# Kernel tuning notes

Measured on AMD Instinct MI355X. Metric: run time of the kernel, lower is better.

## Reference

```python
import jax, jax.numpy as jnp
import numpy as np

N_NODES = 50000
N_GRAPHS = 64


def _gcn_layer(x, w, b, src, dst, dinv):
    # GCNConv: out = D^{-1/2} (A+I) D^{-1/2} (x W) + b; self-loops already in src/dst
    xw = x @ w                                  # [N, out]
    norm = (dinv[src] * dinv[dst])[:, None]     # [E+N, 1]
    msgs = xw[src] * norm                       # gather + scale
    out = jax.ops.segment_sum(msgs, dst, num_segments=N_NODES)
    return out + b


def setup_inputs() -> dict:
    key = jax.random.key(0)
    ks = jax.random.split(key, 12)
    E = 800000
    F_IN, H = 128, 256
    x = jax.random.normal(ks[0], (N_NODES, F_IN), dtype=jnp.float32)
    edge_attr = jax.random.normal(ks[1], (E, 4), dtype=jnp.float32)
    edge_index = jax.random.randint(ks[2], (2, E), 0, N_NODES, dtype=jnp.int64)
    batch = jnp.sort(jax.random.randint(ks[3], (N_NODES,), 0, N_GRAPHS, dtype=jnp.int64))
    def glorot(k, fi, fo):
        s = jnp.sqrt(6.0 / (fi + fo))
        return jax.random.uniform(k, (fi, fo), minval=-s, maxval=s, dtype=jnp.float32)
    return {
        "x": x, "edge_attr": edge_attr, "edge_index": edge_index, "batch": batch,
        "w1": glorot(ks[4], F_IN, H), "b1": jnp.zeros((H,), jnp.float32),
        "w2": glorot(ks[5], H, H), "b2": jnp.zeros((H,), jnp.float32),
        "w3": glorot(ks[6], H, H), "b3": jnp.zeros((H,), jnp.float32),
        "lin1_w": glorot(ks[7], H, H // 2), "lin1_b": jnp.zeros((H // 2,), jnp.float32),
        "lin2_w": glorot(ks[8], H // 2, 3), "lin2_b": jnp.zeros((3,), jnp.float32),
    }


def reference(x, edge_attr, edge_index, batch, w1, b1, w2, b2, w3, b3,
              lin1_w, lin1_b, lin2_w, lin2_b):
    # add self-loops once; shared by all three conv layers
    loop = jnp.arange(N_NODES, dtype=edge_index.dtype)
    src = jnp.concatenate([edge_index[0], loop])
    dst = jnp.concatenate([edge_index[1], loop])
    deg = jax.ops.segment_sum(jnp.ones_like(dst, dtype=x.dtype), dst, num_segments=N_NODES)
    dinv = jnp.where(deg > 0, jax.lax.rsqrt(deg), 0.0)

    h = jax.nn.relu(_gcn_layer(x, w1, b1, src, dst, dinv))
    h = jax.nn.relu(_gcn_layer(h, w2, b2, src, dst, dinv))
    h = _gcn_layer(h, w3, b3, src, dst, dinv)

    # global mean pool over graphs
    sums = jax.ops.segment_sum(h, batch, num_segments=N_GRAPHS)
    cnts = jax.ops.segment_sum(jnp.ones((h.shape[0],), h.dtype), batch, num_segments=N_GRAPHS)
    pooled = sums / jnp.maximum(cnts, 1.0)[:, None]

    # eval mode: dropout is identity
    out = pooled @ lin1_w + lin1_b
    out = out @ lin2_w + lin2_b
    return out
```

## Files before the change

### kernel.cpp

```cpp
#include <hip/hip_runtime.h>
#include <cstdint>

constexpr int NG = 64;
constexpr int H  = 256;

__device__ __forceinline__ uint32_t pk_bf16(float a, float b) {
    uint32_t ua = __builtin_bit_cast(uint32_t, a);
    uint32_t ub = __builtin_bit_cast(uint32_t, b);
    ua += 0x7fffu + ((ua >> 16) & 1u);
    ub += 0x7fffu + ((ub >> 16) & 1u);
    return (ua >> 16) | (ub & 0xffff0000u);
}
__device__ __forceinline__ void bf2acc(uint32_t u, float& a0, float& a1) {
    a0 += __builtin_bit_cast(float, u << 16);
    a1 += __builtin_bit_cast(float, u & 0xffff0000u);
}

__global__ void hist_kernel(const int* __restrict__ dst, int* __restrict__ cnt, int E) {
    int e = blockIdx.x * blockDim.x + threadIdx.x;
    if (e < E) atomicAdd(&cnt[dst[e]], 1);
}

__global__ void dinv_kernel(const int* __restrict__ cnt, float* __restrict__ dinv, int n) {
    int i = blockIdx.x * blockDim.x + threadIdx.x;
    if (i < n) dinv[i] = rsqrtf((float)(cnt[i] + 1));
}

__global__ __launch_bounds__(256) void scanA(const int* __restrict__ cnt, int* __restrict__ bsum, int n) {
    __shared__ int sh[256];
    int t = threadIdx.x, i = blockIdx.x * 256 + t;
    sh[t] = (i < n) ? cnt[i] : 0;
    __syncthreads();
    for (int off = 128; off > 0; off >>= 1) {
        if (t < off) sh[t] += sh[t + off];
        __syncthreads();
    }
    if (t == 0) bsum[blockIdx.x] = sh[0];
}

__global__ __launch_bounds__(256) void scanB(const int* __restrict__ bsum, int* __restrict__ boff,
                                             int* __restrict__ total_out, int nb) {
    __shared__ int sh[256];
    int t = threadIdx.x;
    int v = (t < nb) ? bsum[t] : 0;
    sh[t] = v;
    __syncthreads();
    for (int off = 1; off < 256; off <<= 1) {
        int a = (t >= off) ? sh[t - off] : 0;
        __syncthreads();
        sh[t] += a;
        __syncthreads();
    }
    if (t < nb) boff[t] = sh[t] - v;
    if (t == nb - 1) *total_out = sh[t];
}

__global__ __launch_bounds__(256) void scanC(const int* __restrict__ cnt, const int* __restrict__ boff,
                                             int* __restrict__ row_ptr, int* __restrict__ fill, int n) {
    __shared__ int sh[256];
    int t = threadIdx.x, i = blockIdx.x * 256 + t;
    int v = (i < n) ? cnt[i] : 0;
    sh[t] = v;
    __syncthreads();
    for (int off = 1; off < 256; off <<= 1) {
        int a = (t >= off) ? sh[t - off] : 0;
        __syncthreads();
        sh[t] += a;
        __syncthreads();
    }
    if (i < n) {
        int excl = boff[blockIdx.x] + sh[t] - v;
        row_ptr[i] = excl;
        fill[i] = excl;
    }
}

__global__ void scatter_kernel(const int* __restrict__ src, const int* __restrict__ dst,
                               int* __restrict__ fill, int* __restrict__ ssrc, int E) {
    int e = blockIdx.x * blockDim.x + threadIdx.x;
    if (e < E) {
        int pos = atomicAdd(&fill[dst[e]], 1);
        ssrc[pos] = src[e];
    }
}

__global__ void prescale_kernel(const float* __restrict__ x, const float* __restrict__ dinv,
                                ushort* __restrict__ y, int total ) {
    int idx = blockIdx.x * blockDim.x + threadIdx.x;
    int f = idx * 4;
    if (f >= total) return;
    float dv = dinv[f >> 7];
    float4 v = *reinterpret_cast<const float4*>(x + f);
    uint2 o;
    o.x = pk_bf16(v.x * dv, v.y * dv);
    o.y = pk_bf16(v.z * dv, v.w * dv);
    *reinterpret_cast<uint2*>(y + f) = o;
}

template<int VEC>
__global__ __launch_bounds__(256) void agg_kernel(const ushort* __restrict__ y,
                                                  const float* __restrict__ dinv,
                                                  const int* __restrict__ row_ptr,
                                                  const int* __restrict__ ssrc,
                                                  float* __restrict__ z, int n) {
    constexpr int W = VEC * 64;
    int wave = threadIdx.x >> 6;
    int lane = threadIdx.x & 63;
    int node = blockIdx.x * 4 + wave;
    if (node >= n) return;
    float acc[VEC] = {};

    auto ld4 = [&](int s) -> uint2 {
        return *reinterpret_cast<const uint2*>(y + (size_t)s * W + lane * VEC);
    };
    auto ld2 = [&](int s) -> uint32_t {
        return *reinterpret_cast<const uint32_t*>(y + (size_t)s * W + lane * VEC);
    };

    if constexpr (VEC == 4) {
        uint2 v = ld4(node);
        bf2acc(v.x, acc[0], acc[1]); bf2acc(v.y, acc[2], acc[3]);
    } else {
        bf2acc(ld2(node), acc[0], acc[1]);
    }

    int beg = row_ptr[node], end = row_ptr[node + 1];
    int e = beg;
    for (; e + 4 <= end; e += 4) {
        int s0 = ssrc[e], s1 = ssrc[e + 1], s2 = ssrc[e + 2], s3 = ssrc[e + 3];
        if constexpr (VEC == 4) {
            uint2 v0 = ld4(s0), v1 = ld4(s1), v2 = ld4(s2), v3 = ld4(s3);
            bf2acc(v0.x, acc[0], acc[1]); bf2acc(v0.y, acc[2], acc[3]);
            bf2acc(v1.x, acc[0], acc[1]); bf2acc(v1.y, acc[2], acc[3]);
            bf2acc(v2.x, acc[0], acc[1]); bf2acc(v2.y, acc[2], acc[3]);
            bf2acc(v3.x, acc[0], acc[1]); bf2acc(v3.y, acc[2], acc[3]);
        } else {
            uint32_t v0 = ld2(s0), v1 = ld2(s1), v2 = ld2(s2), v3 = ld2(s3);
            bf2acc(v0, acc[0], acc[1]); bf2acc(v1, acc[0], acc[1]);
            bf2acc(v2, acc[0], acc[1]); bf2acc(v3, acc[0], acc[1]);
        }
    }
    for (; e < end; ++e) {
        if constexpr (VEC == 4) {
            uint2 v = ld4(ssrc[e]);
            bf2acc(v.x, acc[0], acc[1]); bf2acc(v.y, acc[2], acc[3]);
        } else {
            bf2acc(ld2(ssrc[e]), acc[0], acc[1]);
        }
    }

    float dv = dinv[node];
    float* zr = z + (size_t)node * W + lane * VEC;
    if constexpr (VEC == 4) {
        float4 o; o.x = dv * acc[0]; o.y = dv * acc[1]; o.z = dv * acc[2]; o.w = dv * acc[3];
        *reinterpret_cast<float4*>(zr) = o;
    } else {
        float2 o; o.x = dv * acc[0]; o.y = dv * acc[1];
        *reinterpret_cast<float2*>(zr) = o;
    }
}

template<bool RELU>
__global__ __launch_bounds__(256) void gemm_kernel(const float* __restrict__ A,
                                                   const float* __restrict__ Wm,
                                                   const float* __restrict__ bias,
                                                   const float* __restrict__ dinv,
                                                   ushort* __restrict__ C, int M, int K) {
    constexpr int BM = 64, BN = 64, BK = 32;
    __shared__ float As[BK][BM + 4];
    __shared__ float Bs[BK][BN];
    const int tid = threadIdx.x;
    const int bm = blockIdx.x * BM;
    const int bn = blockIdx.y * BN;
    const int tr = tid >> 4;
    const int tc = tid & 15;
    float acc[4][4] = {};
    for (int k0 = 0; k0 < K; k0 += BK) {
        #pragma unroll
        for (int i = tid; i < (BM * BK) / 4; i += 256) {
            int r = i >> 3;
            int c = (i & 7) << 2;
            float4 v = make_float4(0.f, 0.f, 0.f, 0.f);
            int grow = bm + r;
            if (grow < M) v = *reinterpret_cast<const float4*>(A + (size_t)grow * K + k0 + c);
            As[c + 0][r] = v.x; As[c + 1][r] = v.y; As[c + 2][r] = v.z; As[c + 3][r] = v.w;
        }
        #pragma unroll
        for (int i = tid; i < (BK * BN) / 4; i += 256) {
            int r = i >> 4;
            int c = (i & 15) << 2;
            *reinterpret_cast<float4*>(&Bs[r][c]) =
                *reinterpret_cast<const float4*>(Wm + (size_t)(k0 + r) * H + bn + c);
        }
        __syncthreads();
        #pragma unroll
        for (int kk = 0; kk < BK; ++kk) {
            float4 a = *reinterpret_cast<const float4*>(&As[kk][tr * 4]);
            float4 b = *reinterpret_cast<const float4*>(&Bs[kk][tc * 4]);
            float av[4] = {a.x, a.y, a.z, a.w};
            float bv[4] = {b.x, b.y, b.z, b.w};
            #pragma unroll
            for (int i = 0; i < 4; ++i)
                #pragma unroll
                for (int j = 0; j < 4; ++j)
                    acc[i][j] += av[i] * bv[j];
        }
        __syncthreads();
    }
    float4 bvals = *reinterpret_cast<const float4*>(bias + bn + tc * 4);
    float bb[4] = {bvals.x, bvals.y, bvals.z, bvals.w};
    #pragma unroll
    for (int i = 0; i < 4; ++i) {
        int row = bm + tr * 4 + i;
        if (row >= M) continue;
        float dv = dinv[row];
        float t0 = acc[i][0] + bb[0], t1 = acc[i][1] + bb[1];
        float t2 = acc[i][2] + bb[2], t3 = acc[i][3] + bb[3];
        if (RELU) { t0 = fmaxf(t0, 0.f); t1 = fmaxf(t1, 0.f); t2 = fmaxf(t2, 0.f); t3 = fmaxf(t3, 0.f); }
        uint2 o;
        o.x = pk_bf16(t0 * dv, t1 * dv);
        o.y = pk_bf16(t2 * dv, t3 * dv);
        *reinterpret_cast<uint2*>(C + (size_t)row * H + bn + tc * 4) = o;
    }
}

__global__ __launch_bounds__(256) void pool_kernel(const float* __restrict__ z,
                                                   const int* __restrict__ batch,
                                                   float* __restrict__ sums,
                                                   int* __restrict__ gcnt, int n) {
    constexpr int NCH = 128;
    int t = threadIdx.x;
    int base = blockIdx.x * NCH;
    if (base >= n) return;
    int endn = min(base + NCH, n);
    int cur = batch[base];
    float local = 0.f;
    int cl = 0;
    for (int i = base; i < endn; ++i) {
        int g = batch[i];
        if (g != cur) {
            atomicAdd(&sums[cur * H + t], local);
            if (t == 0) atomicAdd(&gcnt[cur], cl);
            local = 0.f; cl = 0; cur = g;
        }
        local += z[(size_t)i * H + t];
        cl++;
    }
    atomicAdd(&sums[cur * H + t], local);
    if (t == 0) atomicAdd(&gcnt[cur], cl);
}

__global__ __launch_bounds__(256) void head_kernel(const float* __restrict__ sums,
                                                   const int* __restrict__ gcnt,
                                                   const float* __restrict__ w3, const float* __restrict__ b3,
                                                   const float* __restrict__ l1w, const float* __restrict__ l1b,
                                                   const float* __restrict__ l2w, const float* __restrict__ l2b,
                                                   float* __restrict__ out) {
    __shared__ float pooled[H];
    __shared__ float t3[H];
    __shared__ float mid[H / 2];
    int g = blockIdx.x, t = threadIdx.x;
    float c = (float)max(gcnt[g], 1);
    pooled[t] = sums[g * H + t] / c;
    __syncthreads();
    float a = b3[t];
    for (int k = 0; k < H; ++k) a += pooled[k] * w3[k * H + t];
    t3[t] = a;
    __syncthreads();
    if (t < H / 2) {
        float m = l1b[t];
        for (int k = 0; k < H; ++k) m += t3[k] * l1w[k * (H / 2) + t];
        mid[t] = m;
    }
    __syncthreads();
    if (t < 3) {
        float o = l2b[t];
        for (int k = 0; k < H / 2; ++k) o += mid[k] * l2w[k * 3 + t];
        out[g * 3 + t] = o;
    }
}

extern "C" void kernel_launch(void* const* d_in, const int* in_sizes, int n_in,
                              void* d_out, int out_size, void* d_ws, size_t ws_size,
                              hipStream_t stream) {
    const float* x   = (const float*)d_in[0];
    const int*   ei  = (const int*)d_in[2];
    const int*   bat = (const int*)d_in[3];
    const float* w1  = (const float*)d_in[4];
    const float* b1  = (const float*)d_in[5];
    const float* w2  = (const float*)d_in[6];
    const float* b2  = (const float*)d_in[7];
    const float* w3  = (const float*)d_in[8];
    const float* b3  = (const float*)d_in[9];
    const float* l1w = (const float*)d_in[10];
    const float* l1b = (const float*)d_in[11];
    const float* l2w = (const float*)d_in[12];
    const float* l2b = (const float*)d_in[13];
    float* out = (float*)d_out;

    const int N = in_sizes[0] / 128;
    const int E = in_sizes[2] / 2;
    const int NB = (N + 255) / 256;

    char* ws = (char*)d_ws;
    size_t off = 0;
    auto alloc = [&](size_t bytes) {
        void* p = ws + off;
        off = (off + bytes + 255) & ~(size_t)255;
        return p;
    };
    ushort* yb     = (ushort*)alloc((size_t)N * H * 2);
    float*  z      = (float*)alloc((size_t)N * H * 4);
    int*    cnt    = (int*)alloc((size_t)N * 4);
    float*  dinv   = (float*)alloc((size_t)N * 4);
    int*    row_ptr= (int*)alloc((size_t)(N + 1) * 4);
    int*    fill   = (int*)alloc((size_t)N * 4);
    int*    ssrc   = (int*)alloc((size_t)E * 4);
    int*    bsum   = (int*)alloc(256 * 4);
    int*    boff   = (int*)alloc(256 * 4);
    float*  sums   = (float*)alloc((size_t)NG * H * 4);
    int*    gcnt   = (int*)alloc((size_t)NG * 4);

    hipMemsetAsync(cnt, 0, (size_t)N * 4, stream);
    hipMemsetAsync(sums, 0, (size_t)NG * H * 4, stream);
    hipMemsetAsync(gcnt, 0, (size_t)NG * 4, stream);

    hist_kernel<<<(E + 255) / 256, 256, 0, stream>>>(ei + E, cnt, E);
    dinv_kernel<<<(N + 255) / 256, 256, 0, stream>>>(cnt, dinv, N);
    scanA<<<NB, 256, 0, stream>>>(cnt, bsum, N);
    scanB<<<1, 256, 0, stream>>>(bsum, boff, row_ptr + N, NB);
    scanC<<<NB, 256, 0, stream>>>(cnt, boff, row_ptr, fill, N);
    scatter_kernel<<<(E + 255) / 256, 256, 0, stream>>>(ei, ei + E, fill, ssrc, E);

    prescale_kernel<<<(N * 128 / 4 + 255) / 256, 256, 0, stream>>>(x, dinv, yb, N * 128);
    agg_kernel<2><<<(N + 3) / 4, 256, 0, stream>>>(yb, dinv, row_ptr, ssrc, z, N);
    gemm_kernel<true><<<dim3((N + 63) / 64, 4), 256, 0, stream>>>(z, w1, b1, dinv, yb, N, 128);

    agg_kernel<4><<<(N + 3) / 4, 256, 0, stream>>>(yb, dinv, row_ptr, ssrc, z, N);
    gemm_kernel<true><<<dim3((N + 63) / 64, 4), 256, 0, stream>>>(z, w2, b2, dinv, yb, N, 256);

    agg_kernel<4><<<(N + 3) / 4, 256, 0, stream>>>(yb, dinv, row_ptr, ssrc, z, N);

    pool_kernel<<<(N + 127) / 128, 256, 0, stream>>>(z, bat, sums, gcnt, N);
    head_kernel<<<NG, 256, 0, stream>>>(sums, gcnt, w3, b3, l1w, l1b, l2w, l2b, out);
}
```

Baseline: 553.8 us.

## Use bf16 MFMA GEMM with split hi/lo weights and bf16 aggregation output

Replaces the fp32 SIMT GEMM with an MFMA 16x16x32 bf16 kernel. Weights are split into bf16 hi and lo parts (transposed) so the weight side keeps near-fp32 precision. Aggregation outputs and pool input move from fp32 to bf16, which halves the intermediate z traffic. The added cost is two small weight conversion kernels, a precision loss on the activations, and per-element scalar bf16 stores in the GEMM epilogue.

```diff
diff --git a/kernel.cpp b/kernel.cpp
--- a/kernel.cpp
+++ b/kernel.cpp
@@ -3,6 +3,9 @@
 
 constexpr int NG = 64;
 constexpr int H  = 256;
+
+typedef __bf16 bf16x8 __attribute__((ext_vector_type(8)));
+typedef float  f32x4  __attribute__((ext_vector_type(4)));
 
 __device__ __forceinline__ uint32_t pk_bf16(float a, float b) {
     uint32_t ua = __builtin_bit_cast(uint32_t, a);
@@ -11,6 +14,14 @@
     ub += 0x7fffu + ((ub >> 16) & 1u);
     return (ua >> 16) | (ub & 0xffff0000u);
 }
+__device__ __forceinline__ ushort bf16r(float x) {
+    uint32_t u = __builtin_bit_cast(uint32_t, x);
+    u += 0x7fffu + ((u >> 16) & 1u);
+    return (ushort)(u >> 16);
+}
+__device__ __forceinline__ float bf2f(ushort h) {
+    return __builtin_bit_cast(float, ((uint32_t)h) << 16);
+}
 __device__ __forceinline__ void bf2acc(uint32_t u, float& a0, float& a1) {
     a0 += __builtin_bit_cast(float, u << 16);
     a1 += __builtin_bit_cast(float, u & 0xffff0000u);
@@ -84,8 +95,20 @@
     }
 }
 
+__global__ void wconv_kernel(const float* __restrict__ w, ushort* __restrict__ hi,
+                             ushort* __restrict__ lo, int K) {
+    int idx = blockIdx.x * 256 + threadIdx.x;
+    if (idx >= K * 256) return;
+    int k = idx >> 8, n = idx & 255;
+    float v = w[idx];
+    ushort h = bf16r(v);
+    float r = v - bf2f(h);
+    hi[n * K + k] = h;
+    lo[n * K + k] = bf16r(r);
+}
+
 __global__ void prescale_kernel(const float* __restrict__ x, const float* __restrict__ dinv,
-                                ushort* __restrict__ y, int total ) {
+                                ushort* __restrict__ y, int total) {
     int idx = blockIdx.x * blockDim.x + threadIdx.x;
     int f = idx * 4;
     if (f >= total) return;
@@ -102,7 +125,7 @@
                                                   const float* __restrict__ dinv,
                                                   const int* __restrict__ row_ptr,
                                                   const int* __restrict__ ssrc,
-                                                  float* __restrict__ z, int n) {
+                                                  ushort* __restrict__ zout, int n) {
     constexpr int W = VEC * 64;
     int wave = threadIdx.x >> 6;
     int lane = threadIdx.x & 63;
@@ -150,81 +173,90 @@
     }
 
     float dv = dinv[node];
-    float* zr = z + (size_t)node * W + lane * VEC;
+    ushort* zp = zout + (size_t)node * W + lane * VEC;
     if constexpr (VEC == 4) {
-        float4 o; o.x = dv * acc[0]; o.y = dv * acc[1]; o.z = dv * acc[2]; o.w = dv * acc[3];
-        *reinterpret_cast<float4*>(zr) = o;
+        uint2 o;
+        o.x = pk_bf16(dv * acc[0], dv * acc[1]);
+        o.y = pk_bf16(dv * acc[2], dv * acc[3]);
+        *reinterpret_cast<uint2*>(zp) = o;
     } else {
-        float2 o; o.x = dv * acc[0]; o.y = dv * acc[1];
-        *reinterpret_cast<float2*>(zr) = o;
+        *reinterpret_cast<uint32_t*>(zp) = pk_bf16(dv * acc[0], dv * acc[1]);
     }
 }
 
 template<bool RELU>
-__global__ __launch_bounds__(256) void gemm_kernel(const float* __restrict__ A,
-                                                   const float* __restrict__ Wm,
-                                                   const float* __restrict__ bias,
-                                                   const float* __restrict__ dinv,
-                                                   ushort* __restrict__ C, int M, int K) {
-    constexpr int BM = 64, BN = 64, BK = 32;
-    __shared__ float As[BK][BM + 4];
-    __shared__ float Bs[BK][BN];
+__global__ __launch_bounds__(256) void mfma_gemm(const ushort* __restrict__ A,
+                                                 const ushort* __restrict__ Bhi,
+                                                 const ushort* __restrict__ Blo,
+                                                 const float* __restrict__ bias,
+                                                 const float* __restrict__ dinv,
+                                                 ushort* __restrict__ C, int M, int K) {
+    constexpr int BM = 64, BN = 64, BK = 64;
+    constexpr int LDK = BK + 8;
+    __shared__ ushort As[BM][LDK];
+    __shared__ ushort Bh[BN][LDK];
+    __shared__ ushort Bl[BN][LDK];
+
     const int tid = threadIdx.x;
+    const int w = tid >> 6;
+    const int l = tid & 63;
+    const int lr = l & 15;
+    const int lk = (l >> 4) * 8;
     const int bm = blockIdx.x * BM;
     const int bn = blockIdx.y * BN;
-    const int tr = tid >> 4;
-    const int tc = tid & 15;
-    float acc[4][4] = {};
+
+    f32x4 acc[4];
+    #pragma unroll
+    for (int i = 0; i < 4; ++i) acc[i] = (f32x4){0.f, 0.f, 0.f, 0.f};
+
     for (int k0 = 0; k0 < K; k0 += BK) {
         #pragma unroll
-        for (int i = tid; i < (BM * BK) / 4; i += 256) {
-            int r = i >> 3;
-            int c = (i & 7) << 2;
-            float4 v = make_float4(0.f, 0.f, 0.f, 0.f);
+        for (int p = 0; p < 2; ++p) {
+            int g = tid + p * 256;
+            int r = g >> 3;
+            int c = (g & 7) << 3;
             int grow = bm + r;
-            if (grow < M) v = *reinterpret_cast<const float4*>(A + (size_t)grow * K + k0 + c);
-            As[c + 0][r] = v.x; As[c + 1][r] = v.y; As[c + 2][r] = v.z; As[c + 3][r] = v.w;
-        }
+            uint4 va = make_uint4(0u, 0u, 0u, 0u);
+            if (grow < M) va = *reinterpret_cast<const uint4*>(A + (size_t)grow * K + k0 + c);
+            *reinterpret_cast<uint4*>(&As[r][c]) = va;
+            *reinterpret_cast<uint4*>(&Bh[r][c]) =
+                *reinterpret_cast<const uint4*>(Bhi + (size_t)(bn + r) * K + k0 + c);
+            *reinterpret_cast<uint4*>(&Bl[r][c]) =
+                *reinterpret_cast<const uint4*>(Blo + (size_t)(bn + r) * K + k0 + c);
+        }
+        __syncthreads();
         #pragma unroll
-        for (int i = tid; i < (BK * BN) / 4; i += 256) {
-            int r = i >> 4;
-            int c = (i & 15) << 2;
-            *reinterpret_cast<float4*>(&Bs[r][c]) =
-                *reinterpret_cast<const float4*>(Wm + (size_t)(k0 + r) * H + bn + c);
-        }
-        __syncthreads();
+        for (int kk = 0; kk < BK; kk += 32) {
+            bf16x8 bh = *reinterpret_cast<const bf16x8*>(&Bh[w * 16 + lr][kk + lk]);
+            bf16x8 bl = *reinterpret_cast<const bf16x8*>(&Bl[w * 16 + lr][kk + lk]);
+            #pragma unroll
+            for (int r16 = 0; r16 < 4; ++r16) {
+                bf16x8 a = *reinterpret_cast<const bf16x8*>(&As[r16 * 16 + lr][kk + lk]);
+                acc[r16] = __builtin_amdgcn_mfma_f32_16x16x32_bf16(a, bh, acc[r16], 0, 0, 0);
+                acc[r16] = __builtin_amdgcn_mfma_f32_16x16x32_bf16(a, bl, acc[r16], 0, 0, 0);
+            }
+        }
+        __syncthreads();
+    }
+
+    int col = bn + w * 16 + lr;
+    float bv = bias[col];
+    #pragma unroll
+    for (int r16 = 0; r16 < 4; ++r16) {
         #pragma unroll
-        for (int kk = 0; kk < BK; ++kk) {
-            float4 a = *reinterpret_cast<const float4*>(&As[kk][tr * 4]);
-            float4 b = *reinterpret_cast<const float4*>(&Bs[kk][tc * 4]);
-            float av[4] = {a.x, a.y, a.z, a.w};
-            float bv[4] = {b.x, b.y, b.z, b.w};
-            #pragma unroll
-            for (int i = 0; i < 4; ++i)
-                #pragma unroll
-                for (int j = 0; j < 4; ++j)
-                    acc[i][j] += av[i] * bv[j];
-        }
-        __syncthreads();
-    }
-    float4 bvals = *reinterpret_cast<const float4*>(bias + bn + tc * 4);
-    float bb[4] = {bvals.x, bvals.y, bvals.z, bvals.w};
-    #pragma unroll
-    for (int i = 0; i < 4; ++i) {
-        int row = bm + tr * 4 + i;
-        if (row >= M) continue;
-        float dv = dinv[row];
-        float t0 = acc[i][0] + bb[0], t1 = acc[i][1] + bb[1];
-        float t2 = acc[i][2] + bb[2], t3 = acc[i][3] + bb[3];
-        if (RELU) { t0 = fmaxf(t0, 0.f); t1 = fmaxf(t1, 0.f); t2 = fmaxf(t2, 0.f); t3 = fmaxf(t3, 0.f); }
-        uint2 o;
-        o.x = pk_bf16(t0 * dv, t1 * dv);
-        o.y = pk_bf16(t2 * dv, t3 * dv);
-        *reinterpret_cast<uint2*>(C + (size_t)row * H + bn + tc * 4) = o;
-    }
-}
-
-__global__ __launch_bounds__(256) void pool_kernel(const float* __restrict__ z,
+        for (int j = 0; j < 4; ++j) {
+            int row = bm + r16 * 16 + (l >> 4) * 4 + j;
+            if (row < M) {
+                float v = acc[r16][j] + bv;
+                if (RELU) v = fmaxf(v, 0.f);
+                v *= dinv[row];
+                C[(size_t)row * H + col] = bf16r(v);
+            }
+        }
+    }
+}
+
+__global__ __launch_bounds__(256) void pool_kernel(const ushort* __restrict__ z,
                                                    const int* __restrict__ batch,
                                                    float* __restrict__ sums,
                                                    int* __restrict__ gcnt, int n) {
@@ -243,7 +275,7 @@
             if (t == 0) atomicAdd(&gcnt[cur], cl);
             local = 0.f; cl = 0; cur = g;
         }
-        local += z[(size_t)i * H + t];
+        local += bf2f(z[(size_t)i * H + t]);
         cl++;
     }
     atomicAdd(&sums[cur * H + t], local);
@@ -310,7 +342,7 @@
         return p;
     };
     ushort* yb     = (ushort*)alloc((size_t)N * H * 2);
-    float*  z      = (float*)alloc((size_t)N * H * 4);
+    ushort* z16    = (ushort*)alloc((size_t)N * H * 2);
     int*    cnt    = (int*)alloc((size_t)N * 4);
     float*  dinv   = (float*)alloc((size_t)N * 4);
     int*    row_ptr= (int*)alloc((size_t)(N + 1) * 4);
@@ -318,6 +350,10 @@
     int*    ssrc   = (int*)alloc((size_t)E * 4);
     int*    bsum   = (int*)alloc(256 * 4);
     int*    boff   = (int*)alloc(256 * 4);
+    ushort* wt1h   = (ushort*)alloc((size_t)128 * 256 * 2);
+    ushort* wt1l   = (ushort*)alloc((size_t)128 * 256 * 2);
+    ushort* wt2h   = (ushort*)alloc((size_t)256 * 256 * 2);
+    ushort* wt2l   = (ushort*)alloc((size_t)256 * 256 * 2);
     float*  sums   = (float*)alloc((size_t)NG * H * 4);
     int*    gcnt   = (int*)alloc((size_t)NG * 4);
 
@@ -332,15 +368,18 @@
     scanC<<<NB, 256, 0, stream>>>(cnt, boff, row_ptr, fill, N);
     scatter_kernel<<<(E + 255) / 256, 256, 0, stream>>>(ei, ei + E, fill, ssrc, E);
 
+    wconv_kernel<<<(128 * 256) / 256, 256, 0, stream>>>(w1, wt1h, wt1l, 128);
+    wconv_kernel<<<(256 * 256) / 256, 256, 0, stream>>>(w2, wt2h, wt2l, 256);
+
     prescale_kernel<<<(N * 128 / 4 + 255) / 256, 256, 0, stream>>>(x, dinv, yb, N * 128);
-    agg_kernel<2><<<(N + 3) / 4, 256, 0, stream>>>(yb, dinv, row_ptr, ssrc, z, N);
-    gemm_kernel<true><<<dim3((N + 63) / 64, 4), 256, 0, stream>>>(z, w1, b1, dinv, yb, N, 128);
-
-    agg_kernel<4><<<(N + 3) / 4, 256, 0, stream>>>(yb, dinv, row_ptr, ssrc, z, N);
-    gemm_kernel<true><<<dim3((N + 63) / 64, 4), 256, 0, stream>>>(z, w2, b2, dinv, yb, N, 256);
-
-    agg_kernel<4><<<(N + 3) / 4, 256, 0, stream>>>(yb, dinv, row_ptr, ssrc, z, N);
-
-    pool_kernel<<<(N + 127) / 128, 256, 0, stream>>>(z, bat, sums, gcnt, N);
+    agg_kernel<2><<<(N + 3) / 4, 256, 0, stream>>>(yb, dinv, row_ptr, ssrc, z16, N);
+    mfma_gemm<true><<<dim3((N + 63) / 64, 4), 256, 0, stream>>>(z16, wt1h, wt1l, b1, dinv, yb, N, 128);
+
+    agg_kernel<4><<<(N + 3) / 4, 256, 0, stream>>>(yb, dinv, row_ptr, ssrc, z16, N);
+    mfma_gemm<true><<<dim3((N + 63) / 64, 4), 256, 0, stream>>>(z16, wt2h, wt2l, b2, dinv, yb, N, 256);
+
+    agg_kernel<4><<<(N + 3) / 4, 256, 0, stream>>>(yb, dinv, row_ptr, ssrc, z16, N);
+
+    pool_kernel<<<(N + 127) / 128, 256, 0, stream>>>(z16, bat, sums, gcnt, N);
     head_kernel<<<NG, 256, 0, stream>>>(sums, gcnt, w3, b3, l1w, l1b, l2w, l2b, out);
 }
```

Measured after the change: 486.0 us. 12.2% less time.
